# Kernel tuning notes

Hardware: AMD Instinct MI355X
Metric: run time of the kernel (lower is better)

The kernel has to match this reference:

```python
import jax, jax.numpy as jnp
import numpy as np

EMBED_DIM = 1024
HEAD_DIM = 64
BATCH = 2
SEQ = 4096


def setup_inputs() -> dict:
    key = jax.random.key(0)
    kx, kq, kk, kv = jax.random.split(key, 4)
    x = jax.random.normal(kx, (BATCH, SEQ, EMBED_DIM), dtype=jnp.float32)
    # nn.Linear(embedding_dim, head_dim, bias=False) weights, stored as [in, out]
    s = 1.0 / np.sqrt(EMBED_DIM)
    Wq = jax.random.uniform(kq, (EMBED_DIM, HEAD_DIM), jnp.float32, -s, s)
    Wk = jax.random.uniform(kk, (EMBED_DIM, HEAD_DIM), jnp.float32, -s, s)
    Wv = jax.random.uniform(kv, (EMBED_DIM, HEAD_DIM), jnp.float32, -s, s)
    return {"x": x, "Wq": Wq, "Wk": Wk, "Wv": Wv}


def reference(x, Wq, Wk, Wv):
    # x: [B, S, E]
    Q = x @ Wq  # [B, S, D]
    K = x @ Wk
    V = x @ Wv
    seq_len = Q.shape[1]
    head_dim = Q.shape[2]
    scores = jnp.einsum('bsd,btd->bst', Q, K) / jnp.sqrt(jnp.float32(head_dim))
    # Original adds a mask that is 1.0 on the causal (lower-tri) positions and
    # -inf elsewhere (tril(ones) with zeros replaced by -inf). The +1 on allowed
    # positions is a uniform row shift, but we keep it for bitwise faithfulness.
    causal = jnp.tril(jnp.ones((seq_len, seq_len), dtype=scores.dtype))
    mask = jnp.where(causal == 0, -jnp.inf, causal)
    scores = scores + mask  # [B, S, S]
    attn = jax.nn.softmax(scores, axis=-1)
    return jnp.einsum('bst,btd->bsd', attn, V)  # [B, S, D]
```

## Files before the change

kernel.cpp:

```cpp
#include <hip/hip_runtime.h>
#include <hip/hip_bf16.h>


typedef short short8 __attribute__((ext_vector_type(8)));
typedef float f32x4 __attribute__((ext_vector_type(4)));
typedef float f32x16 __attribute__((ext_vector_type(16)));
typedef unsigned int uint4e __attribute__((ext_vector_type(4)));
typedef unsigned short ushort4e __attribute__((ext_vector_type(4)));

#define NEGINF (-3.0e38f)
#define SCQ 0.18033688011112042f

static __device__ __forceinline__ unsigned short f2bf(float f) {
  __hip_bfloat16 h = __float2bfloat16(f);
  return __builtin_bit_cast(unsigned short, h);
}
static __device__ __forceinline__ f32x16 mfma32(short8 a, short8 b, f32x16 c) {
  return __builtin_amdgcn_mfma_f32_32x32x16_bf16(a, b, c, 0, 0, 0);
}

__global__ __launch_bounds__(256) void wprep_kernel(
    const float* __restrict__ Wq, const float* __restrict__ Wk,
    const float* __restrict__ Wv, unsigned short* __restrict__ Wt) {
  int w = blockIdx.x >> 3;
  int kc = blockIdx.x & 7;
  int k0 = kc * 128;
  const float* W = (w == 0) ? Wq : ((w == 1) ? Wk : Wv);
  float sc = (w == 0) ? SCQ : 1.0f;

  __shared__ unsigned short lt[128][66];
#pragma unroll
  for (int i = 0; i < 32; ++i) {
    int e = i * 256 + threadIdx.x;
    int k = e >> 6, n = e & 63;
    lt[k][n] = f2bf(W[(size_t)(k0 + k) * 64 + n] * sc);
  }
  __syncthreads();
#pragma unroll
  for (int i = 0; i < 32; ++i) {
    int e = i * 256 + threadIdx.x;
    int n = e >> 7, k = e & 127;
    Wt[(size_t)(w * 64 + n) * 1024 + k0 + k] = lt[k][n];
  }
}

__global__ __launch_bounds__(256, 2) void qkv_proj_kernel(
    const float* __restrict__ x, const unsigned short* __restrict__ Wt,
    unsigned short* __restrict__ Qb, unsigned short* __restrict__ Kb,
    unsigned short* __restrict__ Vt) {
  int lane = threadIdx.x & 63;
  int w = threadIdx.x >> 6;
  int r = lane & 15;
  int hi = lane >> 4;
  int sbase = blockIdx.x * 16;

  __shared__ alignas(16) float lds_part[4][3072];

  const float* xp = x + (size_t)(sbase + r) * 1024 + w * 256 + hi * 8;

  f32x4 acc[12];
#pragma unroll
  for (int t = 0; t < 12; ++t)
#pragma unroll
    for (int i = 0; i < 4; ++i) acc[t][i] = 0.f;

  f32x4 a0 = *(const f32x4*)(xp);
  f32x4 a1 = *(const f32x4*)(xp + 4);
#pragma unroll
  for (int k0 = 0; k0 < 256; k0 += 32) {
    short8 af;
#pragma unroll
    for (int j = 0; j < 4; ++j) {
      af[j] = (short)f2bf(a0[j]);
      af[4 + j] = (short)f2bf(a1[j]);
    }
    if (k0 + 32 < 256) {
      a0 = *(const f32x4*)(xp + k0 + 32);
      a1 = *(const f32x4*)(xp + k0 + 36);
    }
    const unsigned short* wb = Wt + (size_t)r * 1024 + w * 256 + k0 + hi * 8;
#pragma unroll
    for (int t = 0; t < 12; ++t) {
      short8 bf = *(const short8*)(wb + (size_t)((t >> 2) * 64 + (t & 3) * 16) * 1024);
      acc[t] = __builtin_amdgcn_mfma_f32_16x16x32_bf16(af, bf, acc[t], 0, 0, 0);
    }
  }

  float* lp = lds_part[w];
#pragma unroll
  for (int t = 0; t < 12; ++t)
#pragma unroll
    for (int v = 0; v < 4; ++v)
      lp[t * 256 + (hi * 4 + v) * 16 + r] = acc[t][v];
  __syncthreads();

#pragma unroll
  for (int i = 0; i < 2; ++i) {
    int task = threadIdx.x + i * 256;
    int t = task >> 6;
    int off = (task & 63) * 4;
    f32x4 s = *(const f32x4*)(&lds_part[0][t * 256 + off]);
    s += *(const f32x4*)(&lds_part[1][t * 256 + off]);
    s += *(const f32x4*)(&lds_part[2][t * 256 + off]);
    s += *(const f32x4*)(&lds_part[3][t * 256 + off]);
    int row = off >> 4, c0 = off & 15;
    ushort4e pk;
#pragma unroll
    for (int j = 0; j < 4; ++j) pk[j] = f2bf(s[j]);
    unsigned short* dst = (t < 4) ? Qb : Kb;
    *(ushort4e*)(dst + (size_t)(sbase + row) * 64 + (t & 3) * 16 + c0) = pk;
  }
  {
    int t = 8 + (threadIdx.x >> 6);
    int col = (threadIdx.x >> 2) & 15;
    int rg = threadIdx.x & 3;
    ushort4e pk;
#pragma unroll
    for (int j = 0; j < 4; ++j) {
      int idx = t * 256 + (rg * 4 + j) * 16 + col;
      float s = lds_part[0][idx] + lds_part[1][idx] + lds_part[2][idx] + lds_part[3][idx];
      pk[j] = f2bf(s);
    }
    int d = (t - 8) * 16 + col;
    int bidx = sbase >> 12, so = sbase & 4095;
    *(ushort4e*)(Vt + ((size_t)(bidx * 64 + d)) * 4096 + so + rg * 4) = pk;
  }
}

__global__ __launch_bounds__(256, 2) void attn_kernel(
    const unsigned short* __restrict__ Qb, const unsigned short* __restrict__ Kb,
    const unsigned short* __restrict__ Vt, float* __restrict__ Opart,
    float* __restrict__ Mpart, float* __restrict__ Lpart) {
  int bid = blockIdx.x;
  int q = 127 - (bid >> 3);
  int b = (bid >> 2) & 1;
  int hh = bid & 3;
  int lane = threadIdx.x & 63;
  int p = threadIdx.x >> 6;
  int g = hh * 4 + p;
  int ql = lane & 31;
  int h = lane >> 5;
  int sbase = q * 32;

  __shared__ float sm[4][32];
  __shared__ float sl[4][32];
  __shared__ alignas(16) float Op[4][32][68];

  const unsigned short* Qp = Qb + ((size_t)(b * 4096 + sbase + ql)) * 64 + h * 8;
  short8 qf0 = *(const short8*)(Qp);
  short8 qf1 = *(const short8*)(Qp + 16);
  short8 qf2 = *(const short8*)(Qp + 32);
  short8 qf3 = *(const short8*)(Qp + 48);

  f32x16 o0, o1;
#pragma unroll
  for (int i = 0; i < 16; ++i) { o0[i] = 0.f; o1[i] = 0.f; }
  float m = NEGINF, l = 0.f;

  int npairs = (q + 2) >> 1;
  const unsigned short* Kbb = Kb + (size_t)b * 4096 * 64;
  const unsigned short* Vbb = Vt + ((size_t)(b * 64 + ql)) * 4096 + h * 8;

  short8 k0a, k0b, k0c, k0d, k1a, k1b, k1c, k1d;
  {
    const unsigned short* Kp = Kbb + (size_t)(g * 64 + ql) * 64 + h * 8;
    k0a = *(const short8*)(Kp);
    k0b = *(const short8*)(Kp + 16);
    k0c = *(const short8*)(Kp + 32);
    k0d = *(const short8*)(Kp + 48);
    k1a = *(const short8*)(Kp + 2048);
    k1b = *(const short8*)(Kp + 2048 + 16);
    k1c = *(const short8*)(Kp + 2048 + 32);
    k1d = *(const short8*)(Kp + 2048 + 48);
  }

  for (int j = g; j < npairs; j += 16) {
    int kbase = j * 64;
    const unsigned short* Vp = Vbb + kbase;
    short8 vf0 = *(const short8*)(Vp);
    short8 vf1 = *(const short8*)(Vp + 16);
    short8 vf2 = *(const short8*)(Vp + 32);
    short8 vf3 = *(const short8*)(Vp + 48);
    short8 vg0 = *(const short8*)(Vp + 32 * 4096);
    short8 vg1 = *(const short8*)(Vp + 32 * 4096 + 16);
    short8 vg2 = *(const short8*)(Vp + 32 * 4096 + 32);
    short8 vg3 = *(const short8*)(Vp + 32 * 4096 + 48);

    f32x16 st0, st1;
#pragma unroll
    for (int i = 0; i < 16; ++i) { st0[i] = 0.f; st1[i] = 0.f; }
    __builtin_amdgcn_s_setprio(1);
    st0 = mfma32(k0a, qf0, st0);
    st0 = mfma32(k0b, qf1, st0);
    st0 = mfma32(k0c, qf2, st0);
    st0 = mfma32(k0d, qf3, st0);
    st1 = mfma32(k1a, qf0, st1);
    st1 = mfma32(k1b, qf1, st1);
    st1 = mfma32(k1c, qf2, st1);
    st1 = mfma32(k1d, qf3, st1);
    __builtin_amdgcn_s_setprio(0);

    if (j + 16 < npairs) {
      const unsigned short* Kp = Kbb + (size_t)((j + 16) * 64 + ql) * 64 + h * 8;
      k0a = *(const short8*)(Kp);
      k0b = *(const short8*)(Kp + 16);
      k0c = *(const short8*)(Kp + 32);
      k0d = *(const short8*)(Kp + 48);
      k1a = *(const short8*)(Kp + 2048);
      k1b = *(const short8*)(Kp + 2048 + 16);
      k1c = *(const short8*)(Kp + 2048 + 32);
      k1d = *(const short8*)(Kp + 2048 + 48);
    }

    if (2 * j == q) {
#pragma unroll
      for (int rg = 0; rg < 16; ++rg) {
        int kvl = (rg & 3) + 8 * (rg >> 2) + 4 * h;
        if (kvl > ql) st0[rg] = NEGINF;
        st1[rg] = NEGINF;
      }
    } else if (2 * j + 1 == q) {
#pragma unroll
      for (int rg = 0; rg < 16; ++rg) {
        int kvl = (rg & 3) + 8 * (rg >> 2) + 4 * h;
        if (kvl > ql) st1[rg] = NEGINF;
      }
    }

    float mx[16];
#pragma unroll
    for (int i = 0; i < 16; ++i) mx[i] = fmaxf(st0[i], st1[i]);
#pragma unroll
    for (int s = 8; s >= 1; s >>= 1)
#pragma unroll
      for (int i = 0; i < s; ++i) mx[i] = fmaxf(mx[i], mx[i + s]);
    float tm = fmaxf(mx[0], __shfl_xor(mx[0], 32));
    float nm = fmaxf(m, tm);
    float alpha = exp2f(m - nm);
#pragma unroll
    for (int i = 0; i < 16; ++i) {
      st0[i] = exp2f(st0[i] - nm);
      st1[i] = exp2f(st1[i] - nm);
    }
    float sv[16];
#pragma unroll
    for (int i = 0; i < 16; ++i) sv[i] = st0[i] + st1[i];
#pragma unroll
    for (int s = 8; s >= 1; s >>= 1)
#pragma unroll
      for (int i = 0; i < s; ++i) sv[i] += sv[i + s];
    float sum = sv[0] + __shfl_xor(sv[0], 32);
    l = l * alpha + sum;
    m = nm;
#pragma unroll
    for (int i = 0; i < 16; ++i) { o0[i] *= alpha; o1[i] *= alpha; }

    unsigned int pw0[8], pw1[8], sw0[8], sw1[8];
#pragma unroll
    for (int t = 0; t < 8; ++t) {
      pw0[t] = (unsigned int)f2bf(st0[2 * t]) | ((unsigned int)f2bf(st0[2 * t + 1]) << 16);
      pw1[t] = (unsigned int)f2bf(st1[2 * t]) | ((unsigned int)f2bf(st1[2 * t + 1]) << 16);
    }
#pragma unroll
    for (int t = 0; t < 8; ++t) {
      sw0[t] = __shfl_xor(pw0[t], 32);
      sw1[t] = __shfl_xor(pw1[t], 32);
    }
    uint4e bw0 = {h ? sw0[2] : pw0[0], h ? sw0[3] : pw0[1], h ? pw0[2] : sw0[0], h ? pw0[3] : sw0[1]};
    uint4e bw1 = {h ? sw0[6] : pw0[4], h ? sw0[7] : pw0[5], h ? pw0[6] : sw0[4], h ? pw0[7] : sw0[5]};
    uint4e bw2 = {h ? sw1[2] : pw1[0], h ? sw1[3] : pw1[1], h ? pw1[2] : sw1[0], h ? pw1[3] : sw1[1]};
    uint4e bw3 = {h ? sw1[6] : pw1[4], h ? sw1[7] : pw1[5], h ? pw1[6] : sw1[4], h ? pw1[7] : sw1[5]};
    short8 pb0 = __builtin_bit_cast(short8, bw0);
    short8 pb1 = __builtin_bit_cast(short8, bw1);
    short8 pb2 = __builtin_bit_cast(short8, bw2);
    short8 pb3 = __builtin_bit_cast(short8, bw3);

    __builtin_amdgcn_s_setprio(1);
    o0 = mfma32(vf0, pb0, o0);
    o0 = mfma32(vf1, pb1, o0);
    o0 = mfma32(vf2, pb2, o0);
    o0 = mfma32(vf3, pb3, o0);
    o1 = mfma32(vg0, pb0, o1);
    o1 = mfma32(vg1, pb1, o1);
    o1 = mfma32(vg2, pb2, o1);
    o1 = mfma32(vg3, pb3, o1);
    __builtin_amdgcn_s_setprio(0);
  }

  if (h == 0) sm[p][ql] = m;
  __syncthreads();
  float gm = sm[0][ql];
#pragma unroll
  for (int i = 1; i < 4; ++i) gm = fmaxf(gm, sm[i][ql]);
  float alpha = exp2f(m - gm);
  if (h == 0) sl[p][ql] = alpha * l;
  float* Ob = &Op[p][ql][0];
#pragma unroll
  for (int u = 0; u < 4; ++u) {
    f32x4 w0 = {alpha * o0[4 * u], alpha * o0[4 * u + 1], alpha * o0[4 * u + 2], alpha * o0[4 * u + 3]};
    *(f32x4*)(Ob + u * 8 + h * 4) = w0;
    f32x4 w1 = {alpha * o1[4 * u], alpha * o1[4 * u + 1], alpha * o1[4 * u + 2], alpha * o1[4 * u + 3]};
    *(f32x4*)(Ob + 32 + u * 8 + h * 4) = w1;
  }
  __syncthreads();

  float* Od = Opart + (size_t)bid * 2048;
#pragma unroll
  for (int i = 0; i < 2; ++i) {
    int task = threadIdx.x + i * 256;
    int row = task >> 4;
    int c4 = (task & 15) * 4;
    f32x4 accv = *(const f32x4*)(&Op[0][row][c4]);
#pragma unroll
    for (int pp = 1; pp < 4; ++pp) accv += *(const f32x4*)(&Op[pp][row][c4]);
    *(f32x4*)(Od + row * 64 + c4) = accv;
  }
  if (threadIdx.x < 32) {
    int row = threadIdx.x;
    float gmv = fmaxf(fmaxf(sm[0][row], sm[1][row]), fmaxf(sm[2][row], sm[3][row]));
    Mpart[(size_t)bid * 32 + row] = gmv;
    Lpart[(size_t)bid * 32 + row] = sl[0][row] + sl[1][row] + sl[2][row] + sl[3][row];
  }
}

__global__ __launch_bounds__(256) void combine_kernel(
    const float* __restrict__ Opart, const float* __restrict__ Mpart,
    const float* __restrict__ Lpart, float* __restrict__ out) {
  int gid = blockIdx.x * 256 + threadIdx.x;
  int c4 = (gid & 15) * 4;
  int row = gid >> 4;
  int r = row & 31;
  int qg = row >> 5;
  int b = qg >> 7, q = qg & 127;
  int base = (127 - q) * 8 + b * 4;

  float mm[4];
  float gm = NEGINF;
#pragma unroll
  for (int i = 0; i < 4; ++i) {
    mm[i] = Mpart[(size_t)(base + i) * 32 + r];
    gm = fmaxf(gm, mm[i]);
  }
  float L = 0.f;
  f32x4 o = {0.f, 0.f, 0.f, 0.f};
#pragma unroll
  for (int i = 0; i < 4; ++i) {
    float e = exp2f(mm[i] - gm);
    L += e * Lpart[(size_t)(base + i) * 32 + r];
    f32x4 ov = *(const f32x4*)(Opart + (size_t)(base + i) * 2048 + r * 64 + c4);
    o += e * ov;
  }
  float invl = 1.0f / L;
  f32x4 res = {o[0] * invl, o[1] * invl, o[2] * invl, o[3] * invl};
  *(f32x4*)(out + (size_t)row * 64 + c4) = res;
}

extern "C" void kernel_launch(void* const* d_in, const int* in_sizes, int n_in,
                              void* d_out, int out_size, void* d_ws, size_t ws_size,
                              hipStream_t stream) {
  const float* x  = (const float*)d_in[0];
  const float* Wq = (const float*)d_in[1];
  const float* Wk = (const float*)d_in[2];
  const float* Wv = (const float*)d_in[3];
  float* out = (float*)d_out;

  if (ws_size < 12189696) return;

  char* ws = (char*)d_ws;
  unsigned short* Wt = (unsigned short*)(ws + 0);
  unsigned short* Qb = (unsigned short*)(ws + 393216);
  unsigned short* Kb = (unsigned short*)(ws + 1441792);
  unsigned short* Vt = (unsigned short*)(ws + 2490368);
  float* Opart = (float*)(ws + 3538944);
  float* Mpart = (float*)(ws + 11927552);
  float* Lpart = (float*)(ws + 12058624);

  wprep_kernel<<<24, 256, 0, stream>>>(Wq, Wk, Wv, Wt);
  qkv_proj_kernel<<<512, 256, 0, stream>>>(x, Wt, Qb, Kb, Vt);
  attn_kernel<<<1024, 256, 0, stream>>>(Qb, Kb, Vt, Opart, Mpart, Lpart);
  combine_kernel<<<512, 256, 0, stream>>>(Opart, Mpart, Lpart, out);
}
```

Before: 128.1 us.

## Restructure QKV projection into LDS double-buffered K-loop with 32-row tiles

```diff
diff --git a/kernel.cpp b/kernel.cpp
--- a/kernel.cpp
+++ b/kernel.cpp
@@ -3,6 +3,7 @@
 
 
 typedef short short8 __attribute__((ext_vector_type(8)));
+typedef float f32x2 __attribute__((ext_vector_type(2)));
 typedef float f32x4 __attribute__((ext_vector_type(4)));
 typedef float f32x16 __attribute__((ext_vector_type(16)));
 typedef unsigned int uint4e __attribute__((ext_vector_type(4)));
@@ -44,86 +45,94 @@
   }
 }
 
-__global__ __launch_bounds__(256, 2) void qkv_proj_kernel(
+__global__ __launch_bounds__(512) void qkv_proj_kernel(
     const float* __restrict__ x, const unsigned short* __restrict__ Wt,
     unsigned short* __restrict__ Qb, unsigned short* __restrict__ Kb,
     unsigned short* __restrict__ Vt) {
-  int lane = threadIdx.x & 63;
-  int w = threadIdx.x >> 6;
+  int tid = threadIdx.x;
+  int lane = tid & 63;
+  int wv = tid >> 6;
+  int rt = wv >> 2;
+  int cg = wv & 3;
   int r = lane & 15;
   int hi = lane >> 4;
-  int sbase = blockIdx.x * 16;
-
-  __shared__ alignas(16) float lds_part[4][3072];
-
-  const float* xp = x + (size_t)(sbase + r) * 1024 + w * 256 + hi * 8;
-
-  f32x4 acc[12];
-#pragma unroll
-  for (int t = 0; t < 12; ++t)
+  int sbase = blockIdx.x * 32;
+
+  __shared__ alignas(16) unsigned short xs[2][32][40];
+  __shared__ alignas(16) unsigned short wsl[2][192][40];
+
+  int xrow = tid >> 4;
+  int xcol = (tid & 15) * 2;
+  int p1 = tid;
+  int p2 = tid + 512;
+  const float* xg = x + (size_t)(sbase + xrow) * 1024 + xcol;
+
+  f32x4 acc[3];
+#pragma unroll
+  for (int t = 0; t < 3; ++t)
 #pragma unroll
     for (int i = 0; i < 4; ++i) acc[t][i] = 0.f;
 
-  f32x4 a0 = *(const f32x4*)(xp);
-  f32x4 a1 = *(const f32x4*)(xp + 4);
-#pragma unroll
-  for (int k0 = 0; k0 < 256; k0 += 32) {
-    short8 af;
-#pragma unroll
-    for (int j = 0; j < 4; ++j) {
-      af[j] = (short)f2bf(a0[j]);
-      af[4 + j] = (short)f2bf(a1[j]);
-    }
-    if (k0 + 32 < 256) {
-      a0 = *(const f32x4*)(xp + k0 + 32);
-      a1 = *(const f32x4*)(xp + k0 + 36);
-    }
-    const unsigned short* wb = Wt + (size_t)r * 1024 + w * 256 + k0 + hi * 8;
-#pragma unroll
-    for (int t = 0; t < 12; ++t) {
-      short8 bf = *(const short8*)(wb + (size_t)((t >> 2) * 64 + (t & 3) * 16) * 1024);
-      acc[t] = __builtin_amdgcn_mfma_f32_16x16x32_bf16(af, bf, acc[t], 0, 0, 0);
-    }
-  }
-
-  float* lp = lds_part[w];
-#pragma unroll
-  for (int t = 0; t < 12; ++t)
-#pragma unroll
-    for (int v = 0; v < 4; ++v)
-      lp[t * 256 + (hi * 4 + v) * 16 + r] = acc[t][v];
+  {
+    f32x2 xv = *(const f32x2*)(xg);
+    unsigned int pk = (unsigned int)f2bf(xv[0]) | ((unsigned int)f2bf(xv[1]) << 16);
+    *(unsigned int*)&xs[0][xrow][xcol] = pk;
+    short8 wva = *(const short8*)(Wt + (size_t)(p1 >> 2) * 1024 + (p1 & 3) * 8);
+    *(short8*)&wsl[0][p1 >> 2][(p1 & 3) * 8] = wva;
+    if (tid < 256) {
+      short8 wvb = *(const short8*)(Wt + (size_t)(p2 >> 2) * 1024 + (p2 & 3) * 8);
+      *(short8*)&wsl[0][p2 >> 2][(p2 & 3) * 8] = wvb;
+    }
+  }
   __syncthreads();
 
-#pragma unroll
-  for (int i = 0; i < 2; ++i) {
-    int task = threadIdx.x + i * 256;
-    int t = task >> 6;
-    int off = (task & 63) * 4;
-    f32x4 s = *(const f32x4*)(&lds_part[0][t * 256 + off]);
-    s += *(const f32x4*)(&lds_part[1][t * 256 + off]);
-    s += *(const f32x4*)(&lds_part[2][t * 256 + off]);
-    s += *(const f32x4*)(&lds_part[3][t * 256 + off]);
-    int row = off >> 4, c0 = off & 15;
-    ushort4e pk;
-#pragma unroll
-    for (int j = 0; j < 4; ++j) pk[j] = f2bf(s[j]);
-    unsigned short* dst = (t < 4) ? Qb : Kb;
-    *(ushort4e*)(dst + (size_t)(sbase + row) * 64 + (t & 3) * 16 + c0) = pk;
-  }
-  {
-    int t = 8 + (threadIdx.x >> 6);
-    int col = (threadIdx.x >> 2) & 15;
-    int rg = threadIdx.x & 3;
-    ushort4e pk;
-#pragma unroll
-    for (int j = 0; j < 4; ++j) {
-      int idx = t * 256 + (rg * 4 + j) * 16 + col;
-      float s = lds_part[0][idx] + lds_part[1][idx] + lds_part[2][idx] + lds_part[3][idx];
-      pk[j] = f2bf(s);
-    }
-    int d = (t - 8) * 16 + col;
-    int bidx = sbase >> 12, so = sbase & 4095;
-    *(ushort4e*)(Vt + ((size_t)(bidx * 64 + d)) * 4096 + so + rg * 4) = pk;
+  for (int c = 0; c < 32; ++c) {
+    int cur = c & 1;
+    bool has_next = (c + 1) < 32;
+    f32x2 xv;
+    short8 wva, wvb;
+    if (has_next) {
+      int k0 = (c + 1) * 32;
+      xv = *(const f32x2*)(xg + k0);
+      wva = *(const short8*)(Wt + (size_t)(p1 >> 2) * 1024 + k0 + (p1 & 3) * 8);
+      if (tid < 256)
+        wvb = *(const short8*)(Wt + (size_t)(p2 >> 2) * 1024 + k0 + (p2 & 3) * 8);
+    }
+    short8 af = *(const short8*)&xs[cur][rt * 16 + r][hi * 8];
+#pragma unroll
+    for (int tt = 0; tt < 3; ++tt) {
+      short8 bf = *(const short8*)&wsl[cur][(cg * 3 + tt) * 16 + r][hi * 8];
+      acc[tt] = __builtin_amdgcn_mfma_f32_16x16x32_bf16(af, bf, acc[tt], 0, 0, 0);
+    }
+    if (has_next) {
+      int nb = cur ^ 1;
+      unsigned int pk = (unsigned int)f2bf(xv[0]) | ((unsigned int)f2bf(xv[1]) << 16);
+      *(unsigned int*)&xs[nb][xrow][xcol] = pk;
+      *(short8*)&wsl[nb][p1 >> 2][(p1 & 3) * 8] = wva;
+      if (tid < 256) *(short8*)&wsl[nb][p2 >> 2][(p2 & 3) * 8] = wvb;
+    }
+    __syncthreads();
+  }
+
+  int lr = rt * 16 + hi * 4;
+#pragma unroll
+  for (int tt = 0; tt < 3; ++tt) {
+    int gt = cg * 3 + tt;
+    if (gt < 8) {
+      unsigned short* dst = (gt < 4) ? Qb : Kb;
+      int col = (gt & 3) * 16 + r;
+#pragma unroll
+      for (int v = 0; v < 4; ++v)
+        dst[(size_t)(sbase + lr + v) * 64 + col] = f2bf(acc[tt][v]);
+    } else {
+      int d = (gt - 8) * 16 + r;
+      ushort4e pk;
+#pragma unroll
+      for (int v = 0; v < 4; ++v) pk[v] = f2bf(acc[tt][v]);
+      int bidx = sbase >> 12;
+      int so = (sbase & 4095) + lr;
+      *(ushort4e*)(Vt + ((size_t)(bidx * 64 + d)) * 4096 + so) = pk;
+    }
   }
 }
 
@@ -376,7 +385,7 @@
   float* Lpart = (float*)(ws + 12058624);
 
   wprep_kernel<<<24, 256, 0, stream>>>(Wq, Wk, Wv, Wt);
-  qkv_proj_kernel<<<512, 256, 0, stream>>>(x, Wt, Qb, Kb, Vt);
+  qkv_proj_kernel<<<256, 512, 0, stream>>>(x, Wt, Qb, Kb, Vt);
   attn_kernel<<<1024, 256, 0, stream>>>(Qb, Kb, Vt, Opart, Mpart, Lpart);
   combine_kernel<<<512, 256, 0, stream>>>(Opart, Mpart, Lpart, out);
 }
```

After: 125.3 us. 1.02x faster.
